# Kernel optimization log

Measured on AMD Instinct MI355X. Metric: run time of the kernel, lower is better.

Reference implementation:

```python
import jax, jax.numpy as jnp
import numpy as np

B, H, V, DEPTH = 64, 1024, 32000, 5


def setup_inputs() -> dict:
    key = jax.random.key(0)
    ks = jax.random.split(key, 9)
    s = 1.0 / np.sqrt(H)
    u = lambda k, shape: jax.random.uniform(k, shape, jnp.float32, -s, s)
    return {
        "encoding": jax.random.normal(ks[0], (B, H), jnp.float32),
        "Whh_l": u(ks[1], (3 * H, H)),
        "bih_l": u(ks[2], (3 * H,)),
        "bhh_l": u(ks[3], (3 * H,)),
        "Whh_r": u(ks[4], (3 * H, H)),
        "bih_r": u(ks[5], (3 * H,)),
        "bhh_r": u(ks[6], (3 * H,)),
        "W_out": u(ks[7], (V, H)),
        "b_out": u(ks[8], (V,)),
        "depth": DEPTH,
    }


def _gru_zero_input(h, Whh, bih, bhh):
    # PyTorch GRU cell with x == 0: W_ih @ x vanishes, only b_ih survives.
    d = h.shape[-1]
    gh = h @ Whh.T + bhh                                   # [N, 3H]
    r = jax.nn.sigmoid(bih[:d] + gh[..., :d])
    z = jax.nn.sigmoid(bih[d:2 * d] + gh[..., d:2 * d])
    n = jnp.tanh(bih[2 * d:] + r * gh[..., 2 * d:])
    return (1.0 - z) * n + z * h


def reference(encoding, Whh_l, bih_l, bhh_l, Whh_r, bih_r, bhh_r, W_out, b_out, depth):
    b, h = encoding.shape
    cur = encoding[:, None, :]                             # [B, 1, H] roots
    for _ in range(depth):                                 # expand perfect binary tree, level-batched
        n = cur.shape[1]
        flat = cur.reshape(b * n, h)
        left = _gru_zero_input(flat, Whh_l, bih_l, bhh_l).reshape(b, n, h)
        right = _gru_zero_input(flat, Whh_r, bih_r, bhh_r).reshape(b, n, h)
        cur = jnp.stack([left, right], axis=2).reshape(b, 2 * n, h)  # interleave children
    logits = jnp.einsum("blh,vh->blv", cur, W_out) + b_out  # [B, L, V]
    return jax.nn.log_softmax(logits, axis=-1)
```

## Files before the change

kernel.cpp:

```cpp
#include <hip/hip_runtime.h>
#include <hip/hip_bf16.h>
#include <cstdint>
#include <cstddef>

#define H_DIM   1024
#define B_DIM   64
#define V_DIM   32000
#define DEPTH_C 5

using bf16x8  = __attribute__((ext_vector_type(8))) __bf16;
using bf16x4  = __attribute__((ext_vector_type(4))) __bf16;
using floatx4 = __attribute__((ext_vector_type(4))) float;

__device__ __forceinline__ void gl_lds16(const __bf16* g, __bf16* l) {
  __builtin_amdgcn_global_load_lds(
      (const __attribute__((address_space(1))) unsigned int*)g,
      (__attribute__((address_space(3))) unsigned int*)l, 16, 0, 0);
}

__global__ __launch_bounds__(256) void f2b(const float* __restrict__ in,
                                           __bf16* __restrict__ out, int n) {
  for (int i = (blockIdx.x * 256 + threadIdx.x) * 4; i < n;
       i += gridDim.x * 1024) {
    float4 v = *(const float4*)(in + i);
    bf16x4 o;
    o[0] = (__bf16)v.x; o[1] = (__bf16)v.y; o[2] = (__bf16)v.z; o[3] = (__bf16)v.w;
    *(bf16x4*)(out + i) = o;
  }
}

__device__ __forceinline__ bf16x8 cvt8(float4 a, float4 b) {
  bf16x8 r;
  r[0] = (__bf16)a.x; r[1] = (__bf16)a.y; r[2] = (__bf16)a.z; r[3] = (__bf16)a.w;
  r[4] = (__bf16)b.x; r[5] = (__bf16)b.y; r[6] = (__bf16)b.z; r[7] = (__bf16)b.w;
  return r;
}

template <int TN, bool LOGITS, bool WBF16>
__global__ __launch_bounds__(256) void gemm_nt(
    const __bf16* __restrict__ A, const __bf16* __restrict__ Wb0,
    const __bf16* __restrict__ Wb1, const float* __restrict__ Wf,
    __bf16* __restrict__ Cb, float* __restrict__ Cf,
    const float* __restrict__ bias, int M, int N) {
  constexpr int K = H_DIM;
  constexpr int MI = (TN == 128) ? 4 : 2;
  __shared__ __align__(16) __bf16 As[128 * 32];
  __shared__ __align__(16) __bf16 Bs[TN * 32];

  const int tid  = threadIdx.x;
  const int m0   = blockIdx.x * 128;
  const int n0   = blockIdx.y * TN;
  const int lane = tid & 63;
  const int wave = tid >> 6;
  const int lrow = lane & 15;
  const int quad = lane >> 4;
  const int wm   = (TN == 128) ? (wave >> 1) * 64 : wave * 32;
  const int wn   = (TN == 128) ? (wave & 1) * 64 : 0;

  const __bf16* Wb = Wb0;
  int nw0 = n0;
  if (!LOGITS && n0 >= 3072) { Wb = Wb1; nw0 = n0 - 3072; }

  const int sr = tid >> 2;
  const int sk = (tid & 3) * 8;

  int ra0 = m0 + sr;      if (ra0 >= M) ra0 = M - 1;
  int ra1 = m0 + sr + 64; if (ra1 >= M) ra1 = M - 1;
  const __bf16* ga0 = A + (size_t)ra0 * K + sk;
  const __bf16* ga1 = A + (size_t)ra1 * K + sk;
  const __bf16* gb0 = nullptr; const __bf16* gb1 = nullptr;
  const float* gf0 = nullptr; const float* gf1 = nullptr;
  if (WBF16) {
    gb0 = Wb + (size_t)(nw0 + sr) * K + sk;
    if (TN == 128) gb1 = Wb + (size_t)(nw0 + sr + 64) * K + sk;
  } else {
    gf0 = Wf + (size_t)(n0 + sr) * K + sk;
    gf1 = Wf + (size_t)(n0 + sr + 64) * K + sk;
  }

  floatx4 acc[MI][4] = {};

  for (int kt = 0; kt < K; kt += 32) {
    float4 w00, w01, w10, w11;
    if (!WBF16) {
      w00 = *(const float4*)(gf0 + kt);
      w01 = *(const float4*)(gf0 + kt + 4);
      w10 = *(const float4*)(gf1 + kt);
      w11 = *(const float4*)(gf1 + kt + 4);
    }
    __syncthreads();
    gl_lds16(ga0 + kt, As + tid * 8);
    gl_lds16(ga1 + kt, As + 2048 + tid * 8);
    if (WBF16) {
      gl_lds16(gb0 + kt, Bs + tid * 8);
      if (TN == 128) gl_lds16(gb1 + kt, Bs + 2048 + tid * 8);
    } else {
      *(bf16x8*)(&Bs[sr * 32 + sk])        = cvt8(w00, w01);
      *(bf16x8*)(&Bs[(sr + 64) * 32 + sk]) = cvt8(w10, w11);
    }
    __syncthreads();

    bf16x8 af[MI], bfr[4];
#pragma unroll
    for (int i = 0; i < MI; i++)
      af[i] = *(const bf16x8*)(&As[(wm + i * 16 + lrow) * 32 + quad * 8]);
#pragma unroll
    for (int j = 0; j < 4; j++)
      bfr[j] = *(const bf16x8*)(&Bs[(wn + j * 16 + lrow) * 32 + quad * 8]);
#pragma unroll
    for (int i = 0; i < MI; i++)
#pragma unroll
      for (int j = 0; j < 4; j++)
        acc[i][j] =
            __builtin_amdgcn_mfma_f32_16x16x32_bf16(af[i], bfr[j], acc[i][j], 0, 0, 0);
  }

#pragma unroll
  for (int i = 0; i < MI; i++) {
#pragma unroll
    for (int j = 0; j < 4; j++) {
      const int col = n0 + wn + j * 16 + lrow;
      const float bv = LOGITS ? bias[col] : 0.0f;
#pragma unroll
      for (int r = 0; r < 4; r++) {
        const int row = m0 + wm + i * 16 + quad * 4 + r;
        if (row < M) {
          if (LOGITS) Cf[(size_t)row * N + col] = acc[i][j][r] + bv;
          else        Cb[(size_t)row * N + col] = (__bf16)acc[i][j][r];
        }
      }
    }
  }
}

__global__ __launch_bounds__(256) void gru_gate(
    const __bf16* __restrict__ gh, const float* __restrict__ bih_l,
    const float* __restrict__ bhh_l, const float* __restrict__ bih_r,
    const float* __restrict__ bhh_r, const __bf16* __restrict__ hin,
    __bf16* __restrict__ hout, int n) {
  const int row = blockIdx.x;
  const int col = blockIdx.y * 256 + threadIdx.x;
  const int b = row / n, j = row - b * n;
  const size_t g6 = (size_t)row * 6144;
  const float hv = (float)hin[(size_t)row * H_DIM + col];
  const size_t obase = (size_t)(b * 2 * n + 2 * j) * H_DIM;

  {
    float gr = (float)gh[g6 + col] + bhh_l[col];
    float gz = (float)gh[g6 + 1024 + col] + bhh_l[1024 + col];
    float gn = (float)gh[g6 + 2048 + col] + bhh_l[2048 + col];
    float r = 1.f / (1.f + __expf(-(bih_l[col] + gr)));
    float z = 1.f / (1.f + __expf(-(bih_l[1024 + col] + gz)));
    float nn = tanhf(bih_l[2048 + col] + r * gn);
    hout[obase + col] = (__bf16)((1.f - z) * nn + z * hv);
  }
  {
    float gr = (float)gh[g6 + 3072 + col] + bhh_r[col];
    float gz = (float)gh[g6 + 4096 + col] + bhh_r[1024 + col];
    float gn = (float)gh[g6 + 5120 + col] + bhh_r[2048 + col];
    float r = 1.f / (1.f + __expf(-(bih_r[col] + gr)));
    float z = 1.f / (1.f + __expf(-(bih_r[1024 + col] + gz)));
    float nn = tanhf(bih_r[2048 + col] + r * gn);
    hout[obase + H_DIM + col] = (__bf16)((1.f - z) * nn + z * hv);
  }
}

__global__ __launch_bounds__(256) void logsoftmax_rows(float* __restrict__ out) {
  const int row = blockIdx.x;
  float4* p4 = (float4*)(out + (size_t)row * V_DIM);
  const int tid = threadIdx.x;

  float m = -3.0e38f, s = 0.f;
  for (int i = tid; i < 8000; i += 256) {
    float4 v = p4[i];
    float cm = fmaxf(fmaxf(v.x, v.y), fmaxf(v.z, v.w));
    if (cm > m) { s *= __expf(m - cm); m = cm; }
    s += __expf(v.x - m) + __expf(v.y - m) + __expf(v.z - m) + __expf(v.w - m);
  }
#pragma unroll
  for (int off = 32; off; off >>= 1) {
    float om = __shfl_xor(m, off, 64);
    float os = __shfl_xor(s, off, 64);
    float nm = fmaxf(m, om);
    s = s * __expf(m - nm) + os * __expf(om - nm);
    m = nm;
  }
  __shared__ float rm[4], rs[4];
  if ((tid & 63) == 0) { rm[tid >> 6] = m; rs[tid >> 6] = s; }
  __syncthreads();
  const float M4 = fmaxf(fmaxf(rm[0], rm[1]), fmaxf(rm[2], rm[3]));
  const float S4 = rs[0] * __expf(rm[0] - M4) + rs[1] * __expf(rm[1] - M4) +
                   rs[2] * __expf(rm[2] - M4) + rs[3] * __expf(rm[3] - M4);
  const float lg = M4 + __logf(S4);
  for (int i = tid; i < 8000; i += 256) {
    float4 v = p4[i];
    v.x -= lg; v.y -= lg; v.z -= lg; v.w -= lg;
    p4[i] = v;
  }
}

extern "C" void kernel_launch(void* const* d_in, const int* in_sizes, int n_in,
                              void* d_out, int out_size, void* d_ws,
                              size_t ws_size, hipStream_t stream) {
  const float* enc   = (const float*)d_in[0];
  const float* Whh_l = (const float*)d_in[1];
  const float* bih_l = (const float*)d_in[2];
  const float* bhh_l = (const float*)d_in[3];
  const float* Whh_r = (const float*)d_in[4];
  const float* bih_r = (const float*)d_in[5];
  const float* bhh_r = (const float*)d_in[6];
  const float* W_out = (const float*)d_in[7];
  const float* b_out = (const float*)d_in[8];
  float* out = (float*)d_out;

  char* ws = (char*)d_ws;
  __bf16* ghb    = (__bf16*)ws;
  __bf16* buf0   = (__bf16*)(ws + 12582912);
  __bf16* buf1   = (__bf16*)(ws + 16777216);
  __bf16* WhhB_l = (__bf16*)(ws + 20971520);
  __bf16* WhhB_r = WhhB_l + 3145728;
  __bf16* encB   = (__bf16*)(ws + 33554432);
  __bf16* WoutB  = (__bf16*)(ws + 33685504);
  const bool big = ws_size >= (size_t)(33685504 + 65536000);

  f2b<<<256, 256, 0, stream>>>(Whh_l, WhhB_l, 3 * H_DIM * H_DIM);
  f2b<<<256, 256, 0, stream>>>(Whh_r, WhhB_r, 3 * H_DIM * H_DIM);
  f2b<<<64, 256, 0, stream>>>(enc, encB, B_DIM * H_DIM);
  if (big) f2b<<<1024, 256, 0, stream>>>(W_out, WoutB, V_DIM * H_DIM);

  const __bf16* cur = encB;
  __bf16* nxt = buf0;
  int n = 1;
  for (int d = 0; d < DEPTH_C; d++) {
    const int M = B_DIM * n;
    dim3 gg((M + 127) / 128, 6144 / 64);
    gemm_nt<64, false, true><<<gg, 256, 0, stream>>>(
        cur, WhhB_l, WhhB_r, nullptr, ghb, nullptr, nullptr, M, 6144);
    gru_gate<<<dim3(M, 4), 256, 0, stream>>>(ghb, bih_l, bhh_l, bih_r, bhh_r,
                                             cur, nxt, n);
    cur = nxt;
    nxt = (nxt == buf0) ? buf1 : buf0;
    n *= 2;
  }

  dim3 gf(2048 / 128, V_DIM / 128);
  if (big)
    gemm_nt<128, true, true><<<gf, 256, 0, stream>>>(
        cur, WoutB, nullptr, nullptr, nullptr, out, b_out, 2048, V_DIM);
  else
    gemm_nt<128, true, false><<<gf, 256, 0, stream>>>(
        cur, nullptr, nullptr, W_out, nullptr, out, b_out, 2048, V_DIM);
  logsoftmax_rows<<<2048, 256, 0, stream>>>(out);
}
```

Before: 818.2 us.

## Fuse log-softmax row statistics into logits GEMM epilogue and swizzle block mapping

The logits GEMM epilogue now computes per-row partial max and sum-of-exp for each 128-column tile and stores them in a partials buffer that reuses the gate workspace. The finishing kernel merges these partials instead of re-reading the full logits matrix for the statistics pass, removing one large memory sweep. Workgroup indices are also remapped across 8 groups, likely to improve cache locality across XCDs. The epilogue adds shuffles, exps and a block barrier to the GEMM.

```diff
diff --git a/kernel.cpp b/kernel.cpp
--- a/kernel.cpp
+++ b/kernel.cpp
@@ -41,15 +41,24 @@
     const __bf16* __restrict__ A, const __bf16* __restrict__ Wb0,
     const __bf16* __restrict__ Wb1, const float* __restrict__ Wf,
     __bf16* __restrict__ Cb, float* __restrict__ Cf,
-    const float* __restrict__ bias, int M, int N) {
+    const float* __restrict__ bias, float2* __restrict__ part, int M, int N) {
   constexpr int K = H_DIM;
   constexpr int MI = (TN == 128) ? 4 : 2;
   __shared__ __align__(16) __bf16 As[128 * 32];
   __shared__ __align__(16) __bf16 Bs[TN * 32];
 
   const int tid  = threadIdx.x;
-  const int m0   = blockIdx.x * 128;
-  const int n0   = blockIdx.y * TN;
+  const int nbx = gridDim.x;
+  const int nwg = nbx * gridDim.y;
+  int hflat = blockIdx.y * nbx + blockIdx.x;
+  if ((nwg & 7) == 0) {
+    const int cpx = nwg >> 3;
+    hflat = (hflat & 7) * cpx + (hflat >> 3);
+  }
+  const int bx = hflat % nbx;
+  const int by = hflat / nbx;
+  const int m0   = bx * 128;
+  const int n0   = by * TN;
   const int lane = tid & 63;
   const int wave = tid >> 6;
   const int lrow = lane & 15;
@@ -115,20 +124,59 @@
             __builtin_amdgcn_mfma_f32_16x16x32_bf16(af[i], bfr[j], acc[i][j], 0, 0, 0);
   }
 
+  float bv[4];
+  if constexpr (LOGITS) {
+#pragma unroll
+    for (int j = 0; j < 4; j++) bv[j] = bias[n0 + wn + j * 16 + lrow];
+  }
 #pragma unroll
   for (int i = 0; i < MI; i++) {
 #pragma unroll
     for (int j = 0; j < 4; j++) {
       const int col = n0 + wn + j * 16 + lrow;
-      const float bv = LOGITS ? bias[col] : 0.0f;
 #pragma unroll
       for (int r = 0; r < 4; r++) {
         const int row = m0 + wm + i * 16 + quad * 4 + r;
         if (row < M) {
-          if (LOGITS) Cf[(size_t)row * N + col] = acc[i][j][r] + bv;
+          if (LOGITS) Cf[(size_t)row * N + col] = acc[i][j][r] + bv[j];
           else        Cb[(size_t)row * N + col] = (__bf16)acc[i][j][r];
         }
       }
+    }
+  }
+
+  if constexpr (LOGITS) {
+    __shared__ float pmax[2][128], psum[2][128];
+    const int wnh = wn >> 6;
+#pragma unroll
+    for (int i = 0; i < MI; i++) {
+#pragma unroll
+      for (int r = 0; r < 4; r++) {
+        float mx = -3.0e38f;
+#pragma unroll
+        for (int j = 0; j < 4; j++) mx = fmaxf(mx, acc[i][j][r] + bv[j]);
+#pragma unroll
+        for (int mask = 1; mask < 16; mask <<= 1)
+          mx = fmaxf(mx, __shfl_xor(mx, mask, 64));
+        float sm = 0.f;
+#pragma unroll
+        for (int j = 0; j < 4; j++) sm += __expf(acc[i][j][r] + bv[j] - mx);
+#pragma unroll
+        for (int mask = 1; mask < 16; mask <<= 1)
+          sm += __shfl_xor(sm, mask, 64);
+        if (lrow == 0) {
+          pmax[wnh][wm + i * 16 + quad * 4 + r] = mx;
+          psum[wnh][wm + i * 16 + quad * 4 + r] = sm;
+        }
+      }
+    }
+    __syncthreads();
+    if (tid < 128) {
+      const float ma = pmax[0][tid], mb = pmax[1][tid];
+      const float nm = fmaxf(ma, mb);
+      const float ns = psum[0][tid] * __expf(ma - nm) +
+                       psum[1][tid] * __expf(mb - nm);
+      part[(size_t)(m0 + tid) * gridDim.y + by] = make_float2(nm, ns);
     }
   }
 }
@@ -165,17 +213,16 @@
   }
 }
 
-__global__ __launch_bounds__(256) void logsoftmax_rows(float* __restrict__ out) {
+__global__ __launch_bounds__(256) void lsm_finish(
+    float* __restrict__ out, const float2* __restrict__ part) {
+  constexpr int NB = V_DIM / 128;
   const int row = blockIdx.x;
-  float4* p4 = (float4*)(out + (size_t)row * V_DIM);
   const int tid = threadIdx.x;
 
   float m = -3.0e38f, s = 0.f;
-  for (int i = tid; i < 8000; i += 256) {
-    float4 v = p4[i];
-    float cm = fmaxf(fmaxf(v.x, v.y), fmaxf(v.z, v.w));
-    if (cm > m) { s *= __expf(m - cm); m = cm; }
-    s += __expf(v.x - m) + __expf(v.y - m) + __expf(v.z - m) + __expf(v.w - m);
+  if (tid < NB) {
+    const float2 p = part[(size_t)row * NB + tid];
+    m = p.x; s = p.y;
   }
 #pragma unroll
   for (int off = 32; off; off >>= 1) {
@@ -192,6 +239,8 @@
   const float S4 = rs[0] * __expf(rm[0] - M4) + rs[1] * __expf(rm[1] - M4) +
                    rs[2] * __expf(rm[2] - M4) + rs[3] * __expf(rm[3] - M4);
   const float lg = M4 + __logf(S4);
+
+  float4* p4 = (float4*)(out + (size_t)row * V_DIM);
   for (int i = tid; i < 8000; i += 256) {
     float4 v = p4[i];
     v.x -= lg; v.y -= lg; v.z -= lg; v.w -= lg;
@@ -221,6 +270,7 @@
   __bf16* WhhB_r = WhhB_l + 3145728;
   __bf16* encB   = (__bf16*)(ws + 33554432);
   __bf16* WoutB  = (__bf16*)(ws + 33685504);
+  float2* part   = (float2*)ghb;
   const bool big = ws_size >= (size_t)(33685504 + 65536000);
 
   f2b<<<256, 256, 0, stream>>>(Whh_l, WhhB_l, 3 * H_DIM * H_DIM);
@@ -235,7 +285,7 @@
     const int M = B_DIM * n;
     dim3 gg((M + 127) / 128, 6144 / 64);
     gemm_nt<64, false, true><<<gg, 256, 0, stream>>>(
-        cur, WhhB_l, WhhB_r, nullptr, ghb, nullptr, nullptr, M, 6144);
+        cur, WhhB_l, WhhB_r, nullptr, ghb, nullptr, nullptr, nullptr, M, 6144);
     gru_gate<<<dim3(M, 4), 256, 0, stream>>>(ghb, bih_l, bhh_l, bih_r, bhh_r,
                                              cur, nxt, n);
     cur = nxt;
@@ -246,9 +296,9 @@
   dim3 gf(2048 / 128, V_DIM / 128);
   if (big)
     gemm_nt<128, true, true><<<gf, 256, 0, stream>>>(
-        cur, WoutB, nullptr, nullptr, nullptr, out, b_out, 2048, V_DIM);
+        cur, WoutB, nullptr, nullptr, nullptr, out, b_out, part, 2048, V_DIM);
   else
     gemm_nt<128, true, false><<<gf, 256, 0, stream>>>(
-        cur, nullptr, nullptr, W_out, nullptr, out, b_out, 2048, V_DIM);
-  logsoftmax_rows<<<2048, 256, 0, stream>>>(out);
-}
+        cur, nullptr, nullptr, W_out, nullptr, out, b_out, part, 2048, V_DIM);
+  lsm_finish<<<2048, 256, 0, stream>>>(out, part);
+}
```

New measurement: 776.7 us. -5.1%, faster.
